# Kernel tuning notes

Measured on AMD Instinct MI355X. Metric: run time of the kernel, lower is better.

## Reference

```python
import jax, jax.numpy as jnp
import numpy as np
from jax import lax

T, B, NI, NH = 512, 64, 512, 512
SIGMA = 0.01


def _rnn_scan(inputs, W_xh, W_hh, b_h, h0):
    # inputs: [T, B, NI]; precompute input projection as one big GEMM
    xw = jnp.einsum('tbi,ih->tbh', inputs, W_xh)  # [T, B, NH]

    def step(h, x):
        h = jnp.tanh(x + h @ W_hh + b_h)
        return h, h

    hT, hs = lax.scan(step, h0, xw)
    return hs, hT  # hs: [T, B, NH]


def setup_inputs() -> dict:
    key = jax.random.key(0)
    ks = jax.random.split(key, 5)
    inputs = jax.random.normal(ks[0], (T, B, NI), dtype=jnp.float32)
    W_xh_f = jax.random.normal(ks[1], (NI, NH), dtype=jnp.float32) * SIGMA
    W_hh_f = jax.random.normal(ks[2], (NH, NH), dtype=jnp.float32) * SIGMA
    b_h_f = jnp.zeros((NH,), dtype=jnp.float32)
    W_xh_b = jax.random.normal(ks[3], (NI, NH), dtype=jnp.float32) * SIGMA
    W_hh_b = jax.random.normal(ks[4], (NH, NH), dtype=jnp.float32) * SIGMA
    b_h_b = jnp.zeros((NH,), dtype=jnp.float32)
    return {"inputs": inputs, "W_xh_f": W_xh_f, "W_hh_f": W_hh_f, "b_h_f": b_h_f,
            "W_xh_b": W_xh_b, "W_hh_b": W_hh_b, "b_h_b": b_h_b}


def reference(inputs, W_xh_f, W_hh_f, b_h_f, W_xh_b, W_hh_b, b_h_b):
    h0 = jnp.zeros((inputs.shape[1], NH), dtype=inputs.dtype)
    f_outs, f_H = _rnn_scan(inputs, W_xh_f, W_hh_f, b_h_f, h0)
    b_outs_rev, b_H = _rnn_scan(inputs[::-1], W_xh_b, W_hh_b, b_h_b, h0)
    b_outs = b_outs_rev[::-1]  # align backward outputs with forward time order
    outputs = jnp.concatenate([f_outs, b_outs], axis=-1)  # [T, B, 2*NH]
    return outputs, f_H, b_H
```

## Files before the change

### kernel.cpp

```cpp
#include <hip/hip_runtime.h>
#include <hip/hip_bf16.h>


typedef __attribute__((ext_vector_type(8))) short short8;
typedef __attribute__((ext_vector_type(4))) float f32x4;
typedef __attribute__((ext_vector_type(4))) int   i32x4;

static __device__ __forceinline__ float bf2f(unsigned short s) {
  return __builtin_bit_cast(float, ((unsigned int)s) << 16);
}
static __device__ __forceinline__ float tanh_cheap(float x) {
  float t = x * 2.8853900817779268f;
  float e;
  asm("v_exp_f32 %0, %1" : "=v"(e) : "v"(t));
  float den = e + 1.0f;
  float r;
  asm("v_rcp_f32 %0, %1" : "=v"(r) : "v"(den));
  return __builtin_fmaf(-2.0f, r, 1.0f);
}
static __device__ __forceinline__ void lds_barrier() {
  __builtin_amdgcn_sched_barrier(0);
  asm volatile("s_waitcnt lgkmcnt(0)" ::: "memory");
  __builtin_amdgcn_s_barrier();
  __builtin_amdgcn_sched_barrier(0);
}
static __device__ __forceinline__ unsigned int cvt_pk_bf16(float a, float b) {
  unsigned int d;
  asm("v_cvt_pk_bf16_f32 %0, %1, %2" : "=v"(d) : "v"(a), "v"(b));
  return d;
}

__global__ __launch_bounds__(256, 4) void xw_gemm(
    const float* __restrict__ inp,
    const float* __restrict__ Wf,
    const float* __restrict__ Wb,
    const float* __restrict__ bhf,
    const float* __restrict__ bhb,
    unsigned short* __restrict__ xwpf,
    unsigned short* __restrict__ xwpb) {
  __shared__ __align__(16) unsigned short As[64 * 40];
  __shared__ __align__(16) unsigned short Bfs[64 * 40];
  __shared__ __align__(16) unsigned short Bbs[64 * 40];
  __shared__ __align__(16) unsigned short CT[2][64][68];
  const int tid = threadIdx.x;
  const int w = tid >> 6, l = tid & 63;
  const int lr = l & 15, lg = l >> 4;
  const int rbase = blockIdx.x * 64;
  const int nbase = blockIdx.y * 64;

  f32x4 accf[4], accb[4];
#pragma unroll
  for (int tn = 0; tn < 4; ++tn) { accf[tn] = (f32x4){0,0,0,0}; accb[tn] = (f32x4){0,0,0,0}; }

  for (int i = 0; i < 16; ++i) {
    const int k0 = i * 32;
    __syncthreads();
#pragma unroll
    for (int e = 0; e < 2; ++e) {
      int lin4 = tid + e * 256;
      int r = lin4 >> 3, c4 = (lin4 & 7) * 4;
      float4 v = *reinterpret_cast<const float4*>(&inp[(rbase + r) * 512 + k0 + c4]);
      uint2 p;
      p.x = cvt_pk_bf16(v.x, v.y);
      p.y = cvt_pk_bf16(v.z, v.w);
      *reinterpret_cast<uint2*>(&As[r * 40 + c4]) = p;
    }
#pragma unroll
    for (int e = 0; e < 2; ++e) {
      int lin4 = tid + e * 256;
      int r = lin4 >> 4, c4 = (lin4 & 15) * 4;
      float4 vf = *reinterpret_cast<const float4*>(&Wf[(k0 + r) * 512 + nbase + c4]);
      float4 vb = *reinterpret_cast<const float4*>(&Wb[(k0 + r) * 512 + nbase + c4]);
      unsigned int uf0 = cvt_pk_bf16(vf.x, vf.y);
      unsigned int uf1 = cvt_pk_bf16(vf.z, vf.w);
      unsigned int ub0 = cvt_pk_bf16(vb.x, vb.y);
      unsigned int ub1 = cvt_pk_bf16(vb.z, vb.w);
      Bfs[(c4 + 0) * 40 + r] = (unsigned short)uf0;
      Bfs[(c4 + 1) * 40 + r] = (unsigned short)(uf0 >> 16);
      Bfs[(c4 + 2) * 40 + r] = (unsigned short)uf1;
      Bfs[(c4 + 3) * 40 + r] = (unsigned short)(uf1 >> 16);
      Bbs[(c4 + 0) * 40 + r] = (unsigned short)ub0;
      Bbs[(c4 + 1) * 40 + r] = (unsigned short)(ub0 >> 16);
      Bbs[(c4 + 2) * 40 + r] = (unsigned short)ub1;
      Bbs[(c4 + 3) * 40 + r] = (unsigned short)(ub1 >> 16);
    }
    __syncthreads();
    const int ar = w * 16 + lr;
    const int kg = lg * 8;
    short8 a = *reinterpret_cast<const short8*>(&As[ar * 40 + kg]);
#pragma unroll
    for (int tn = 0; tn < 4; ++tn) {
      const int bc = tn * 16 + lr;
      short8 bf = *reinterpret_cast<const short8*>(&Bfs[bc * 40 + kg]);
      short8 bb = *reinterpret_cast<const short8*>(&Bbs[bc * 40 + kg]);
      accf[tn] = __builtin_amdgcn_mfma_f32_16x16x32_bf16(a, bf, accf[tn], 0, 0, 0);
      accb[tn] = __builtin_amdgcn_mfma_f32_16x16x32_bf16(a, bb, accb[tn], 0, 0, 0);
    }
  }
  __syncthreads();
#pragma unroll
  for (int tn = 0; tn < 4; ++tn) {
    const int colb = nbase + tn * 16 + lr;
    const float bfv = bhf[colb], bbv = bhb[colb];
    const int gc = tn * 16 + lr;
#pragma unroll
    for (int q = 0; q < 4; ++q) {
      const int gr = w * 16 + lg * 4 + q;
      CT[0][gr][gc] = (unsigned short)cvt_pk_bf16(accf[tn][q] + bfv, 0.f);
      CT[1][gr][gc] = (unsigned short)cvt_pk_bf16(accb[tn][q] + bbv, 0.f);
    }
  }
  __syncthreads();
  unsigned long long* const mats[2] = {
      reinterpret_cast<unsigned long long*>(xwpf),
      reinterpret_cast<unsigned long long*>(xwpb)};
  const int idx0 = tid * 4;
  const int rgl = idx0 >> 8;
  const int wl  = (idx0 >> 7) & 1;
  const int s0  = idx0 & 127;
#pragma unroll
  for (int m = 0; m < 2; ++m) {
    unsigned long long* dst = mats[m] +
        ((((int)blockIdx.x * 4 + rgl) * 16 + (int)blockIdx.y * 2 + wl) * 128) + s0;
#pragma unroll
    for (int e = 0; e < 4; ++e) {
      const int s64 = s0 + e;
      const int ls = s64 >> 1, n = s64 & 1;
      dst[e] = *reinterpret_cast<const unsigned long long*>(
          &CT[m][rgl * 16 + (ls & 15)][wl * 32 + n * 16 + (ls >> 4) * 4]);
    }
  }
}

__global__ __launch_bounds__(1024) void birnn_scan(
    const float* __restrict__ Whf, const float* __restrict__ Whb,
    unsigned short* __restrict__ xwpf, unsigned short* __restrict__ xwpb,
    float* __restrict__ out) {
  const int bid = blockIdx.x;
  const int d  = bid >> 2;
  const int rg = bid & 3;
  const int tid = threadIdx.x;
  const int w = tid >> 6, l = tid & 63;
  const int lr = l & 15, lg = l >> 4;
  const int cbase = w * 32;
  const int rbase = rg * 16;
  const int sx = lr & 7;
  const int ro = lr * 512;

  const float* Wh = d ? Whb : Whf;
  unsigned short* xwp = d ? xwpb : xwpf;

  __shared__ __align__(16) signed char hq[2][16][512];
  signed char* const hqf = &hq[0][0][0];

  const float sW = 127.0f / 0.06f;
  i32x4 wq[2][8];
#pragma unroll
  for (int n = 0; n < 2; ++n) {
    const int col = cbase + n * 16 + lr;
#pragma unroll
    for (int kk = 0; kk < 8; ++kk) {
      i32x4 v;
#pragma unroll
      for (int dw = 0; dw < 4; ++dw) {
        unsigned int pack = 0;
#pragma unroll
        for (int jj = 0; jj < 4; ++jj) {
          const int k = kk * 64 + lg * 16 + dw * 4 + jj;
          float wv = Wh[k * 512 + col] * sW;
          wv = fminf(fmaxf(wv, -127.f), 127.f);
          int q = (int)rintf(wv);
          pack |= ((unsigned int)(q & 0xff)) << (8 * jj);
        }
        v[dw] = (int)pack;
      }
      wq[n][kk] = v;
    }
  }
  const float inv_s = 1.0f / (127.0f * sW);

  short8 xA, xB;
  {
    const int t0 = d ? 511 : 0;
    xA = *reinterpret_cast<const short8*>(
        xwp + (((t0 * 4 + rg) * 16 + w) << 9) + (l << 3));
  }
  {
    const int t1 = d ? 510 : 1;
    xB = *reinterpret_cast<const short8*>(
        xwp + (((t1 * 4 + rg) * 16 + w) << 9) + (l << 3));
  }

  uint4 HP;

#define EPI(N, ACC, U0, U1, FINAL_)                                           \
  {                                                                           \
    float h0_ = tanh_cheap(fmaf((float)(ACC)[0], inv_s, bf2f((unsigned short)X[(N)*4+0]))); \
    float h1_ = tanh_cheap(fmaf((float)(ACC)[1], inv_s, bf2f((unsigned short)X[(N)*4+1]))); \
    float h2_ = tanh_cheap(fmaf((float)(ACC)[2], inv_s, bf2f((unsigned short)X[(N)*4+2]))); \
    float h3_ = tanh_cheap(fmaf((float)(ACC)[3], inv_s, bf2f((unsigned short)X[(N)*4+3]))); \
    int q0_ = (int)rintf(h0_ * 127.f) & 255;                                  \
    int q1_ = (int)rintf(h1_ * 127.f) & 255;                                  \
    int q2_ = (int)rintf(h2_ * 127.f) & 255;                                  \
    int q3_ = (int)rintf(h3_ * 127.f);                                        \
    unsigned int pk_ = (unsigned int)q0_ | ((unsigned int)q1_ << 8) |         \
                       ((unsigned int)q2_ << 16) | ((unsigned int)q3_ << 24); \
    *reinterpret_cast<unsigned int*>(hqf + buf_ * 8192 + ro +                 \
        ((((w * 2 + (N)) ^ sx) << 4) + lg * 4)) = pk_;                        \
    U0 = cvt_pk_bf16(h0_, h1_);                                               \
    U1 = cvt_pk_bf16(h2_, h3_);                                               \
    if (FINAL_) {                                                             \
      float4 fv_; fv_.x = h0_; fv_.y = h1_; fv_.z = h2_; fv_.w = h3_;         \
      *reinterpret_cast<float4*>(out + 33554432 + d * 32768 +                 \
          (rbase + lr) * 512 + cbase + (N) * 16 + lg * 4) = fv_;              \
    }                                                                         \
  }

#define STEP(S, XARG, FINAL_)                                                 \
  do {                                                                        \
    const int s_ = (S);                                                       \
    const int t_ = d ? (511 - s_) : s_;                                       \
    const int buf_ = s_ & 1;                                                  \
    const int pb_ = (s_ - 1) & 1;                                             \
    short8& X = (XARG);                                                       \
    {              \
      const int tp_ = d ? (t_ + 1) : (t_ - 1);                                \
      unsigned short* pw_ = xwp + (((tp_ * 4 + rg) * 16 + w) << 9) + (l << 3);\
      *reinterpret_cast<uint4*>(pw_) = HP;                                    \
    }                                                                         \
    i32x4 acc0 = (i32x4){0,0,0,0}, acc1 = (i32x4){0,0,0,0};                   \
    __builtin_amdgcn_s_setprio(1);                                            \
    {              \
      const signed char* hb_ = hqf + pb_ * 8192 + ro;                         \
      i32x4 a0 = *(const i32x4*)(hb_ + ((((0 * 4 + lg) ^ sx) << 4)));         \
      i32x4 a1 = *(const i32x4*)(hb_ + ((((1 * 4 + lg) ^ sx) << 4)));         \
      i32x4 a2 = *(const i32x4*)(hb_ + ((((2 * 4 + lg) ^ sx) << 4)));         \
      i32x4 a3 = *(const i32x4*)(hb_ + ((((3 * 4 + lg) ^ sx) << 4)));         \
      acc0 = __builtin_amdgcn_mfma_i32_16x16x64_i8(wq[0][0], a0, acc0, 0, 0, 0); \
      acc1 = __builtin_amdgcn_mfma_i32_16x16x64_i8(wq[1][0], a0, acc1, 0, 0, 0); \
      acc0 = __builtin_amdgcn_mfma_i32_16x16x64_i8(wq[0][1], a1, acc0, 0, 0, 0); \
      acc1 = __builtin_amdgcn_mfma_i32_16x16x64_i8(wq[1][1], a1, acc1, 0, 0, 0); \
      acc0 = __builtin_amdgcn_mfma_i32_16x16x64_i8(wq[0][2], a2, acc0, 0, 0, 0); \
      acc1 = __builtin_amdgcn_mfma_i32_16x16x64_i8(wq[1][2], a2, acc1, 0, 0, 0); \
      acc0 = __builtin_amdgcn_mfma_i32_16x16x64_i8(wq[0][3], a3, acc0, 0, 0, 0); \
      acc1 = __builtin_amdgcn_mfma_i32_16x16x64_i8(wq[1][3], a3, acc1, 0, 0, 0); \
    }                                                                         \
    {                                              \
      const signed char* hb_ = hqf + pb_ * 8192 + ro;                         \
      i32x4 a0 = *(const i32x4*)(hb_ + ((((4 * 4 + lg) ^ sx) << 4)));         \
      i32x4 a1 = *(const i32x4*)(hb_ + ((((5 * 4 + lg) ^ sx) << 4)));         \
      i32x4 a2 = *(const i32x4*)(hb_ + ((((6 * 4 + lg) ^ sx) << 4)));         \
      i32x4 a3 = *(const i32x4*)(hb_ + ((((7 * 4 + lg) ^ sx) << 4)));         \
      acc0 = __builtin_amdgcn_mfma_i32_16x16x64_i8(wq[0][4], a0, acc0, 0, 0, 0); \
      acc1 = __builtin_amdgcn_mfma_i32_16x16x64_i8(wq[1][4], a0, acc1, 0, 0, 0); \
      acc0 = __builtin_amdgcn_mfma_i32_16x16x64_i8(wq[0][5], a1, acc0, 0, 0, 0); \
      acc1 = __builtin_amdgcn_mfma_i32_16x16x64_i8(wq[1][5], a1, acc1, 0, 0, 0); \
      acc0 = __builtin_amdgcn_mfma_i32_16x16x64_i8(wq[0][6], a2, acc0, 0, 0, 0); \
      acc1 = __builtin_amdgcn_mfma_i32_16x16x64_i8(wq[1][6], a2, acc1, 0, 0, 0); \
      acc0 = __builtin_amdgcn_mfma_i32_16x16x64_i8(wq[0][7], a3, acc0, 0, 0, 0); \
      acc1 = __builtin_amdgcn_mfma_i32_16x16x64_i8(wq[1][7], a3, acc1, 0, 0, 0); \
    }                                                                         \
    __builtin_amdgcn_s_setprio(0);                                            \
    EPI(0, acc0, HP.x, HP.y, FINAL_);                                         \
    EPI(1, acc1, HP.z, HP.w, FINAL_);                                         \
    {                                    \
      const int tp2_ = d ? (t_ - 2) : (t_ + 2);                               \
      X = *reinterpret_cast<const short8*>(                                   \
          xwp + (((tp2_ * 4 + rg) * 16 + w) << 9) + (l << 3));                \
    }                                                                         \
    lds_barrier();                                                            \
  } while (0)

  {
    const int t_ = d ? 511 : 0;
    const int buf_ = 0;
    short8& X = xA;
    i32x4 z_ = (i32x4){0, 0, 0, 0};
    EPI(0, z_, HP.x, HP.y, 0);
    EPI(1, z_, HP.z, HP.w, 0);
    {
      const int tp2_ = d ? (t_ - 2) : (t_ + 2);
      xA = *reinterpret_cast<const short8*>(
          xwp + (((tp2_ * 4 + rg) * 16 + w) << 9) + (l << 3));
    }
    lds_barrier();
  }

  for (int ss = 0; ss < 255; ++ss) {
    STEP(1 + 2 * ss, xB, 0);
    STEP(2 + 2 * ss, xA, 0);
  }
  STEP(511, xB, 1);

  {
    const int tl_ = d ? 0 : 511;
    unsigned short* pw_ = xwp + (((tl_ * 4 + rg) * 16 + w) << 9) + (l << 3);
    *reinterpret_cast<uint4*>(pw_) = HP;
  }
#undef STEP
#undef EPI
}

__global__ __launch_bounds__(1024) void expand_out(
    const unsigned short* __restrict__ xwpf,
    const unsigned short* __restrict__ xwpb,
    float* __restrict__ out) {
  const int g = blockIdx.x * 1024 + threadIdx.x;
  const int flat = g * 4;
  const int row = flat >> 10;
  const int c   = flat & 1023;
  const int t = row >> 6, b = row & 63;
  const int d = c >> 9, col = c & 511;
  const unsigned long long* buf = reinterpret_cast<const unsigned long long*>(
      d ? xwpb : xwpf);
  const int lidx = ((col >> 2) & 3) * 16 + (b & 15);
  const int chunk = (t * 4 + (b >> 4)) * 16 + (col >> 5);
  unsigned long long hv = buf[chunk * 128 + lidx * 2 + ((col >> 4) & 1)];
  float4 v;
  v.x = bf2f((unsigned short)hv);
  v.y = bf2f((unsigned short)(hv >> 16));
  v.z = bf2f((unsigned short)(hv >> 32));
  v.w = bf2f((unsigned short)(hv >> 48));
  *reinterpret_cast<float4*>(out + flat) = v;
}

extern "C" void kernel_launch(void* const* d_in, const int* in_sizes, int n_in,
                              void* d_out, int out_size, void* d_ws, size_t ws_size,
                              hipStream_t stream) {
  (void)in_sizes; (void)n_in; (void)out_size; (void)ws_size;
  const float* inputs = (const float*)d_in[0];
  const float* W_xh_f = (const float*)d_in[1];
  const float* W_hh_f = (const float*)d_in[2];
  const float* b_h_f  = (const float*)d_in[3];
  const float* W_xh_b = (const float*)d_in[4];
  const float* W_hh_b = (const float*)d_in[5];
  const float* b_h_b  = (const float*)d_in[6];

  unsigned short* xwpf = (unsigned short*)d_ws;
  unsigned short* xwpb = xwpf + 16777216 + 65536;

  dim3 g1(512, 8), b1(256);
  xw_gemm<<<g1, b1, 0, stream>>>(inputs, W_xh_f, W_xh_b, b_h_f, b_h_b, xwpf, xwpb);

  birnn_scan<<<dim3(8), dim3(1024), 0, stream>>>(
      W_hh_f, W_hh_b, xwpf, xwpb, (float*)d_out);

  expand_out<<<dim3(8192), dim3(1024), 0, stream>>>(xwpf, xwpb, (float*)d_out);
}
```

Measured before the change: 851.8 us.

## Write fp32 outputs directly from scan, drop bf16 staging and expand kernel

The scan kernel now stores each step's fp32 hidden state straight into the final output tensor with nontemporal stores. This replaces the bf16 write-back into the xw workspace and removes the separate expand_out kernel. It saves a kernel launch and a read/write pass over the workspace, and outputs keep full fp32 precision instead of bf16. In exchange, the serial scan loop now issues twice as many bytes of global stores per step, on only 8 workgroups, which may slow the latency-bound recurrence.

```diff
diff --git a/kernel.cpp b/kernel.cpp
--- a/kernel.cpp
+++ b/kernel.cpp
@@ -134,7 +134,7 @@
 
 __global__ __launch_bounds__(1024) void birnn_scan(
     const float* __restrict__ Whf, const float* __restrict__ Whb,
-    unsigned short* __restrict__ xwpf, unsigned short* __restrict__ xwpb,
+    const unsigned short* __restrict__ xwpf, const unsigned short* __restrict__ xwpb,
     float* __restrict__ out) {
   const int bid = blockIdx.x;
   const int d  = bid >> 2;
@@ -148,7 +148,7 @@
   const int ro = lr * 512;
 
   const float* Wh = d ? Whb : Whf;
-  unsigned short* xwp = d ? xwpb : xwpf;
+  const unsigned short* xwp = d ? xwpb : xwpf;
 
   __shared__ __align__(16) signed char hq[2][16][512];
   signed char* const hqf = &hq[0][0][0];
@@ -191,9 +191,7 @@
         xwp + (((t1 * 4 + rg) * 16 + w) << 9) + (l << 3));
   }
 
-  uint4 HP;
-
-#define EPI(N, ACC, U0, U1, FINAL_)                                           \
+#define EPI(N, ACC, FINAL_)                                                   \
   {                                                                           \
     float h0_ = tanh_cheap(fmaf((float)(ACC)[0], inv_s, bf2f((unsigned short)X[(N)*4+0]))); \
     float h1_ = tanh_cheap(fmaf((float)(ACC)[1], inv_s, bf2f((unsigned short)X[(N)*4+1]))); \
@@ -207,11 +205,13 @@
                        ((unsigned int)q2_ << 16) | ((unsigned int)q3_ << 24); \
     *reinterpret_cast<unsigned int*>(hqf + buf_ * 8192 + ro +                 \
         ((((w * 2 + (N)) ^ sx) << 4) + lg * 4)) = pk_;                        \
-    U0 = cvt_pk_bf16(h0_, h1_);                                               \
-    U1 = cvt_pk_bf16(h2_, h3_);                                               \
+    f32x4 fv_;                                                                \
+    fv_[0] = h0_; fv_[1] = h1_; fv_[2] = h2_; fv_[3] = h3_;                   \
+    __builtin_nontemporal_store(fv_, reinterpret_cast<f32x4*>(                \
+        out + (t_ * 64 + rbase + lr) * 1024 + d * 512 +                       \
+        cbase + (N) * 16 + lg * 4));                                          \
     if (FINAL_) {                                                             \
-      float4 fv_; fv_.x = h0_; fv_.y = h1_; fv_.z = h2_; fv_.w = h3_;         \
-      *reinterpret_cast<float4*>(out + 33554432 + d * 32768 +                 \
+      *reinterpret_cast<f32x4*>(out + 33554432 + d * 32768 +                  \
           (rbase + lr) * 512 + cbase + (N) * 16 + lg * 4) = fv_;              \
     }                                                                         \
   }
@@ -223,11 +223,6 @@
     const int buf_ = s_ & 1;                                                  \
     const int pb_ = (s_ - 1) & 1;                                             \
     short8& X = (XARG);                                                       \
-    {              \
-      const int tp_ = d ? (t_ + 1) : (t_ - 1);                                \
-      unsigned short* pw_ = xwp + (((tp_ * 4 + rg) * 16 + w) << 9) + (l << 3);\
-      *reinterpret_cast<uint4*>(pw_) = HP;                                    \
-    }                                                                         \
     i32x4 acc0 = (i32x4){0,0,0,0}, acc1 = (i32x4){0,0,0,0};                   \
     __builtin_amdgcn_s_setprio(1);                                            \
     {              \
@@ -261,8 +256,8 @@
       acc1 = __builtin_amdgcn_mfma_i32_16x16x64_i8(wq[1][7], a3, acc1, 0, 0, 0); \
     }                                                                         \
     __builtin_amdgcn_s_setprio(0);                                            \
-    EPI(0, acc0, HP.x, HP.y, FINAL_);                                         \
-    EPI(1, acc1, HP.z, HP.w, FINAL_);                                         \
+    EPI(0, acc0, FINAL_);                                                     \
+    EPI(1, acc1, FINAL_);                                                     \
     {                                    \
       const int tp2_ = d ? (t_ - 2) : (t_ + 2);                               \
       X = *reinterpret_cast<const short8*>(                                   \
@@ -276,8 +271,8 @@
     const int buf_ = 0;
     short8& X = xA;
     i32x4 z_ = (i32x4){0, 0, 0, 0};
-    EPI(0, z_, HP.x, HP.y, 0);
-    EPI(1, z_, HP.z, HP.w, 0);
+    EPI(0, z_, 0);
+    EPI(1, z_, 0);
     {
       const int tp2_ = d ? (t_ - 2) : (t_ + 2);
       xA = *reinterpret_cast<const short8*>(
@@ -291,37 +286,8 @@
     STEP(2 + 2 * ss, xA, 0);
   }
   STEP(511, xB, 1);
-
-  {
-    const int tl_ = d ? 0 : 511;
-    unsigned short* pw_ = xwp + (((tl_ * 4 + rg) * 16 + w) << 9) + (l << 3);
-    *reinterpret_cast<uint4*>(pw_) = HP;
-  }
 #undef STEP
 #undef EPI
-}
-
-__global__ __launch_bounds__(1024) void expand_out(
-    const unsigned short* __restrict__ xwpf,
-    const unsigned short* __restrict__ xwpb,
-    float* __restrict__ out) {
-  const int g = blockIdx.x * 1024 + threadIdx.x;
-  const int flat = g * 4;
-  const int row = flat >> 10;
-  const int c   = flat & 1023;
-  const int t = row >> 6, b = row & 63;
-  const int d = c >> 9, col = c & 511;
-  const unsigned long long* buf = reinterpret_cast<const unsigned long long*>(
-      d ? xwpb : xwpf);
-  const int lidx = ((col >> 2) & 3) * 16 + (b & 15);
-  const int chunk = (t * 4 + (b >> 4)) * 16 + (col >> 5);
-  unsigned long long hv = buf[chunk * 128 + lidx * 2 + ((col >> 4) & 1)];
-  float4 v;
-  v.x = bf2f((unsigned short)hv);
-  v.y = bf2f((unsigned short)(hv >> 16));
-  v.z = bf2f((unsigned short)(hv >> 32));
-  v.w = bf2f((unsigned short)(hv >> 48));
-  *reinterpret_cast<float4*>(out + flat) = v;
 }
 
 extern "C" void kernel_launch(void* const* d_in, const int* in_sizes, int n_in,
@@ -344,6 +310,4 @@
 
   birnn_scan<<<dim3(8), dim3(1024), 0, stream>>>(
       W_hh_f, W_hh_b, xwpf, xwpb, (float*)d_out);
-
-  expand_out<<<dim3(8192), dim3(1024), 0, stream>>>(xwpf, xwpb, (float*)d_out);
-}
+}
```

New measurement: 922.4 us. 1.08x slower.
